# Kernel optimization log

Measured on AMD Instinct MI355X. Metric: run time of the kernel, lower is better.

Reference implementation:

```python
import jax, jax.numpy as jnp
import numpy as np
import math
from itertools import product

IMG = 300
FMAPS = [38, 19, 10, 5, 3, 1]
STEPS = [8, 16, 32, 64, 100, 300]
MINS = [30, 60, 111, 162, 213, 264]
MAXS = [60, 111, 162, 213, 264, 315]
ARS = [[2, 3]] * 6
CHANS = [512, 1024, 512, 256, 256, 256]
NUM_CLASSES = 21
V0, V1 = 0.1, 0.2  # box-encoding variances


def build_priors():
    # faithful port of PriorsBox.forward (runs once, tiny config loop)
    mean = []
    for k, f in enumerate(FMAPS):
        for i, j in product(range(f), repeat=2):
            f_k = IMG / STEPS[k]
            cx = (j + 0.5) / f_k
            cy = (i + 0.5) / f_k
            s_k = MINS[k] / IMG
            mean += [cx, cy, s_k, s_k]
            s_kp = math.sqrt(s_k * (MAXS[k] / IMG))
            mean += [cx, cy, s_kp, s_kp]
            for ar in ARS[k]:
                mean += [cx, cy, s_k * math.sqrt(ar), s_k / math.sqrt(ar)]
                mean += [cx, cy, s_k / math.sqrt(ar), s_k * math.sqrt(ar)]
    p = np.asarray(mean, dtype=np.float32).reshape(-1, 4)
    return np.clip(p, 0.0, 1.0)


def setup_inputs() -> dict:
    key = jax.random.key(0)
    B = 32
    ks = jax.random.split(key, 3 * len(FMAPS))
    inp = {}
    ki = 0
    for s, (C, F) in enumerate(zip(CHANS, FMAPS)):
        inp[f"feat{s}"] = jax.random.normal(ks[ki], (B, C, F, F), jnp.float32); ki += 1
        inp[f"loc_w{s}"] = jax.random.normal(ks[ki], (24, C, 3, 3), jnp.float32) * 0.02; ki += 1
        inp[f"loc_b{s}"] = jnp.zeros((24,), jnp.float32)
        inp[f"conf_w{s}"] = jax.random.normal(ks[ki], (126, C, 3, 3), jnp.float32) * 0.02; ki += 1
        inp[f"conf_b{s}"] = jnp.zeros((126,), jnp.float32)
    inp["priors"] = jnp.asarray(build_priors())  # [11640, 4] cx,cy,w,h
    return inp


def _conv3x3(x, w, b):
    # stride 1, pad 1 -> SAME; NCHW / OIHW layout matches torch Conv2d
    y = jax.lax.conv_general_dilated(x, w, (1, 1), 'SAME',
                                     dimension_numbers=('NCHW', 'OIHW', 'NCHW'))
    return y + b[None, :, None, None]


def _forward(feats, loc_ws, loc_bs, conf_ws, conf_bs, priors):
    B = feats[0].shape[0]
    loc = jnp.concatenate(
        [_conv3x3(x, w, b).transpose(0, 2, 3, 1).reshape(B, -1)
         for x, w, b in zip(feats, loc_ws, loc_bs)], axis=1).reshape(B, -1, 4)
    conf = jnp.concatenate(
        [_conv3x3(x, w, b).transpose(0, 2, 3, 1).reshape(B, -1)
         for x, w, b in zip(feats, conf_ws, conf_bs)], axis=1).reshape(B, -1, NUM_CLASSES)
    scores = jax.nn.softmax(conf, axis=2)
    # decode (vectorized over batch): center-form -> point-form
    p = priors[None]  # [1, P, 4]
    xy = p[..., :2] + loc[..., :2] * V0 * p[..., 2:]
    wh = p[..., 2:] * jnp.exp(loc[..., 2:] * V1)
    mins = xy - wh * 0.5
    boxes = jnp.concatenate([mins, mins + wh], axis=-1)  # [B, P, 4]
    return jnp.concatenate([boxes, scores], axis=-1)  # [B, P, 4 + num_classes]


def reference(feat0, feat1, feat2, feat3, feat4, feat5,
              loc_w0, loc_w1, loc_w2, loc_w3, loc_w4, loc_w5,
              loc_b0, loc_b1, loc_b2, loc_b3, loc_b4, loc_b5,
              conf_w0, conf_w1, conf_w2, conf_w3, conf_w4, conf_w5,
              conf_b0, conf_b1, conf_b2, conf_b3, conf_b4, conf_b5,
              priors):
    feats = (feat0, feat1, feat2, feat3, feat4, feat5)
    loc_ws = (loc_w0, loc_w1, loc_w2, loc_w3, loc_w4, loc_w5)
    loc_bs = (loc_b0, loc_b1, loc_b2, loc_b3, loc_b4, loc_b5)
    conf_ws = (conf_w0, conf_w1, conf_w2, conf_w3, conf_w4, conf_w5)
    conf_bs = (conf_b0, conf_b1, conf_b2, conf_b3, conf_b4, conf_b5)
    return _forward(feats, loc_ws, loc_bs, conf_ws, conf_bs, priors)
```

## Files before the change

### kernel.cpp

```cpp
#include <hip/hip_runtime.h>
#include <hip/hip_bf16.h>
#include <math.h>

typedef __attribute__((ext_vector_type(8))) short bf16x8;
typedef __attribute__((ext_vector_type(16))) float f32x16;

#define NUM_PRIORS 11640
#define OUT_CH 25
#define BATCH 32

#define WT0 0u
#define WT1 1474560u
#define WT2 4423680u
#define WT3 5898240u
#define WT4 6635520u
#define WT5 7372800u
#define XA0 8110080u
#define XA1 60538880u
#define XA2 89440256u
#define XA3 94158848u
#define XA4 94961664u
#define XA5 95371264u
#define CV0 95518720u
#define CV1 125091840u
#define CV2 132485120u
#define CV3 134533120u
#define CV4 135045120u
#define CV5 135229440u
#define WS_TOTAL 135249920u

template <int C>
__device__ __forceinline__
void wprep_body(int idx, const float* lw, const float* cw, unsigned short* wt)
{
  if (idx >= 1440 * C) return;
  constexpr int CK = C / 64;
  const int j    = idx & 7;
  const int lane = (idx >> 3) & 63;
  int rest = idx >> 9;
  const int nt  = rest % 5;  rest /= 5;
  const int ks  = rest & 3;  rest >>= 2;
  const int ck  = rest % CK;
  const int tap = rest / CK;
  const int n = nt * 32 + (lane & 31);
  const int c = ck * 64 + ks * 16 + (lane >> 5) * 8 + j;
  float v = 0.f;
  if (n < 24)       v = lw[((size_t)n        * C + c) * 9 + tap];
  else if (n < 150) v = cw[((size_t)(n - 24) * C + c) * 9 + tap];
  __hip_bfloat16 h = __float2bfloat16(v);
  wt[idx] = *(unsigned short*)&h;
}

template <int C, int F>
__device__ __forceinline__
void xprep_body(int idx, const float* __restrict__ x, unsigned short* __restrict__ xp)
{
  constexpr int P = F + 2, IMGP = P * P, C8 = C / 8, FF = F * F;
  const int pos = idx % IMGP;
  const int bg  = idx / IMGP;
  const int g   = bg % C8;
  const int b   = bg / C8;
  const int py  = pos / P, px = pos % P;
  uint4 out = {0u, 0u, 0u, 0u};
  if (py >= 1 && py <= F && px >= 1 && px <= F) {
    const float* s = x + (((size_t)(b * C + g * 8) * F + (py - 1)) * F + (px - 1));
    unsigned int u[4];
    #pragma unroll
    for (int k = 0; k < 4; ++k) {
      __hip_bfloat162 h = __float22bfloat162_rn(
          float2{s[(size_t)(2 * k) * FF], s[(size_t)(2 * k + 1) * FF]});
      u[k] = *(unsigned int*)&h;
    }
    out.x = u[0]; out.y = u[1]; out.z = u[2]; out.w = u[3];
  }
  *(uint4*)(xp + (size_t)idx * 8) = out;
}

#define XB0 12800
#define XB1 7056
#define XB2 1152
#define XB3 196
#define XB4 100
#define XB5 36
#define WB0 2880
#define WB1 5760
#define WB2 2880
#define WB3 1440
#define WB4 1440
#define WB5 1440
#define PB_TOT (XB0+XB1+XB2+XB3+XB4+XB5+WB0+WB1+WB2+WB3+WB4+WB5)

struct PArgs {
  const float* x[6];
  const float* lw[6];
  const float* cw[6];
  unsigned short* xa[6];
  unsigned short* wt[6];
};

__global__ __launch_bounds__(256)
void prep_all(PArgs a)
{
  int blk = blockIdx.x;
  const int t = threadIdx.x;
  if (blk < XB0) { xprep_body<512, 38>(blk * 256 + t, a.x[0], a.xa[0]); return; } blk -= XB0;
  if (blk < XB1) { xprep_body<1024,19>(blk * 256 + t, a.x[1], a.xa[1]); return; } blk -= XB1;
  if (blk < XB2) { xprep_body<512, 10>(blk * 256 + t, a.x[2], a.xa[2]); return; } blk -= XB2;
  if (blk < XB3) { xprep_body<256,  5>(blk * 256 + t, a.x[3], a.xa[3]); return; } blk -= XB3;
  if (blk < XB4) { xprep_body<256,  3>(blk * 256 + t, a.x[4], a.xa[4]); return; } blk -= XB4;
  if (blk < XB5) { xprep_body<256,  1>(blk * 256 + t, a.x[5], a.xa[5]); return; } blk -= XB5;
  if (blk < WB0) { wprep_body<512> (blk * 256 + t, a.lw[0], a.cw[0], a.wt[0]); return; } blk -= WB0;
  if (blk < WB1) { wprep_body<1024>(blk * 256 + t, a.lw[1], a.cw[1], a.wt[1]); return; } blk -= WB1;
  if (blk < WB2) { wprep_body<512> (blk * 256 + t, a.lw[2], a.cw[2], a.wt[2]); return; } blk -= WB2;
  if (blk < WB3) { wprep_body<256> (blk * 256 + t, a.lw[3], a.cw[3], a.wt[3]); return; } blk -= WB3;
  if (blk < WB4) { wprep_body<256> (blk * 256 + t, a.lw[4], a.cw[4], a.wt[4]); return; } blk -= WB4;
                   wprep_body<256> (blk * 256 + t, a.lw[5], a.cw[5], a.wt[5]);
}

#define BSTEP 2880

template <int C, int F>
__device__ __forceinline__
void conv_body(int bid, int tid, const unsigned short* __restrict__ xp,
               const unsigned short* __restrict__ wt, float* __restrict__ cv,
               uint4 (*lB)[BSTEP])
{
  constexpr int FF   = F * F;
  constexpr int MB   = (FF + 255) / 256;
  constexpr int CK   = C / 64;
  constexpr int P    = F + 2;
  constexpr int IMGP = P * P;
  constexpr int C8   = C / 8;
  constexpr int TS   = CK * 10240;
  constexpr int NIT  = CK * 4;

  const int mt = bid % MB;
  const int b  = bid / MB;

  const int wave = tid >> 6, lane = tid & 63;
  const int mw = wave & 3, ng = wave >> 2;
  const int m0 = mt * 256 + mw * 64;
  const int nbase  = ng * 3;
  const int ncount = ng ? 2 : 3;

  const int cm = lane & 31, khalf = lane >> 5;
  int mi0 = m0 + cm;      if (mi0 > FF - 1) mi0 = FF - 1;
  int mi1 = m0 + 32 + cm; if (mi1 > FF - 1) mi1 = FF - 1;
  const int ay0 = mi0 / F, ax0 = mi0 - ay0 * F;
  const int ay1 = mi1 / F, ax1 = mi1 - ay1 * F;
  const int ylo = m0 / F;
  const int yhi = ((m0 + 63 < FF - 1) ? (m0 + 63) : (FF - 1)) / F;

  const unsigned short* xb = xp + ((size_t)b * C8 + khalf) * IMGP * 8;
  const int o0 = ((ay0 + 1) * P + ax0 + 1) * 8;
  const int o1 = ((ay1 + 1) * P + ax1 + 1) * 8;

  f32x16 acc[2][3];
  #pragma unroll
  for (int mf = 0; mf < 2; ++mf)
    #pragma unroll
    for (int nt = 0; nt < 3; ++nt)
      #pragma unroll
      for (int r = 0; r < 16; ++r) acc[mf][nt][r] = 0.f;

  auto stage = [&](uint4* buf, int it) {
    const int ck = it >> 2, ks = it & 3;
    const unsigned short* wck = wt + ck * 10240 + ks * 2560;
    #pragma unroll
    for (int r = 0; r < 6; ++r) {
      const int e = r * 512 + tid;
      if (r < 5 || e < BSTEP) {
        const int tap = e / 320;
        const int w   = e - tap * 320;
        __builtin_amdgcn_global_load_lds(
            (const __attribute__((address_space(1))) unsigned int*)(wck + (size_t)tap * TS + w * 8),
            (__attribute__((address_space(3))) unsigned int*)&buf[e], 16, 0, 0);
      }
    }
  };

  stage(lB[0], 0);
  int cur = 0;
  #pragma unroll 1
  for (int it = 0; it < NIT; ++it) {
    __syncthreads();
    if (it + 1 < NIT) stage(lB[cur ^ 1], it + 1);
    const int ck = it >> 2, ks = it & 3;
    const unsigned short* xk = xb + (size_t)(ck * 8 + ks * 2) * IMGP * 8;
    const uint4* bp = lB[cur];
    #pragma unroll
    for (int tap = 0; tap < 9; ++tap) {
      const int dy = tap / 3 - 1, dx = tap % 3 - 1;
      if (ylo + dy >= F || yhi + dy < 0) continue;
      if (F == 1 && dx != 0) continue;
      const int d = (dy * P + dx) * 8;
      const bf16x8 a0 = *(const bf16x8*)(xk + o0 + d);
      const bf16x8 a1 = *(const bf16x8*)(xk + o1 + d);
      #pragma unroll
      for (int nt = 0; nt < 3; ++nt) {
        if (nt < ncount) {
          const uint4 u = bp[tap * 320 + (nbase + nt) * 64 + lane];
          const bf16x8 bf = *(const bf16x8*)&u;
          acc[0][nt] = __builtin_amdgcn_mfma_f32_32x32x16_bf16(a0, bf, acc[0][nt], 0, 0, 0);
          acc[1][nt] = __builtin_amdgcn_mfma_f32_32x32x16_bf16(a1, bf, acc[1][nt], 0, 0, 0);
        }
      }
    }
    cur ^= 1;
  }

  float* cb = cv + (size_t)b * FF * 160;
  #pragma unroll
  for (int mf = 0; mf < 2; ++mf)
    #pragma unroll
    for (int nt = 0; nt < 3; ++nt) {
      if (nt < ncount) {
        const int n = (nbase + nt) * 32 + cm;
        #pragma unroll
        for (int r = 0; r < 16; ++r) {
          const int mm = m0 + mf * 32 + (r & 3) + 8 * (r >> 2) + 4 * khalf;
          if (mm < FF) cb[(size_t)mm * 160 + n] = acc[mf][nt][r];
        }
      }
    }
}

#define G1B 64
#define G0B 192
#define G2B 32
#define G3B 32
#define G4B 32
#define G5B 32
#define GB_TOT (G1B + G0B + G2B + G3B + G4B + G5B)

__global__ __launch_bounds__(512, 2)
void gemm_all(char* wsb)
{
  __shared__ uint4 lB[2][BSTEP];
  int blk = blockIdx.x;
  const int tid = threadIdx.x;
  if (blk < G1B) { conv_body<1024,19>(blk, tid, (const unsigned short*)(wsb + XA1),
                                      (const unsigned short*)(wsb + WT1), (float*)(wsb + CV1), lB); return; }
  blk -= G1B;
  if (blk < G0B) { conv_body<512, 38>(blk, tid, (const unsigned short*)(wsb + XA0),
                                      (const unsigned short*)(wsb + WT0), (float*)(wsb + CV0), lB); return; }
  blk -= G0B;
  if (blk < G2B) { conv_body<512, 10>(blk, tid, (const unsigned short*)(wsb + XA2),
                                      (const unsigned short*)(wsb + WT2), (float*)(wsb + CV2), lB); return; }
  blk -= G2B;
  if (blk < G3B) { conv_body<256,  5>(blk, tid, (const unsigned short*)(wsb + XA3),
                                      (const unsigned short*)(wsb + WT3), (float*)(wsb + CV3), lB); return; }
  blk -= G3B;
  if (blk < G4B) { conv_body<256,  3>(blk, tid, (const unsigned short*)(wsb + XA4),
                                      (const unsigned short*)(wsb + WT4), (float*)(wsb + CV4), lB); return; }
  blk -= G4B;
                   conv_body<256,  1>(blk, tid, (const unsigned short*)(wsb + XA5),
                                      (const unsigned short*)(wsb + WT5), (float*)(wsb + CV5), lB);
}

struct DecArgs {
  const float* lb[6];
  const float* cb[6];
};

template <int F>
__device__ __forceinline__
void dec_one(int local, int b, const float* cvs, const float* lb, const float* cb,
             const float* p4, float* o)
{
  constexpr int FF = F * F;
  const int pos = local / 6;
  const int a   = local - pos * 6;
  const float* strip = cvs + ((size_t)b * FF + pos) * 160;

  float cls[21];
  float mx = -1e30f;
  #pragma unroll
  for (int k = 0; k < 21; ++k) {
    cls[k] = strip[24 + a * 21 + k] + cb[a * 21 + k];
    mx = fmaxf(mx, cls[k]);
  }
  float s = 0.f;
  #pragma unroll
  for (int k = 0; k < 21; ++k) { cls[k] = __expf(cls[k] - mx); s += cls[k]; }
  const float inv = 1.f / s;

  const float l0 = strip[a * 4 + 0] + lb[a * 4 + 0];
  const float l1 = strip[a * 4 + 1] + lb[a * 4 + 1];
  const float l2 = strip[a * 4 + 2] + lb[a * 4 + 2];
  const float l3 = strip[a * 4 + 3] + lb[a * 4 + 3];

  const float px = p4[0], py = p4[1], pw = p4[2], ph = p4[3];
  const float cx = px + l0 * 0.1f * pw;
  const float cy = py + l1 * 0.1f * ph;
  const float w  = pw * __expf(l2 * 0.2f);
  const float h  = ph * __expf(l3 * 0.2f);
  const float minx = cx - 0.5f * w;
  const float miny = cy - 0.5f * h;

  o[0] = minx; o[1] = miny; o[2] = minx + w; o[3] = miny + h;
  #pragma unroll
  for (int k = 0; k < 21; ++k) o[4 + k] = cls[k] * inv;
}

__global__ __launch_bounds__(256)
void decode_k(const char* __restrict__ wsb, DecArgs da,
              const float* __restrict__ priors, float* __restrict__ out)
{
  const int gid = blockIdx.x * 256 + threadIdx.x;
  if (gid >= BATCH * NUM_PRIORS) return;
  const int b  = gid / NUM_PRIORS;
  const int pr = gid - b * NUM_PRIORS;
  float* o = out + (size_t)gid * OUT_CH;
  const float* p4 = priors + (size_t)pr * 4;

  if (pr < 8664)       dec_one<38>(pr,         b, (const float*)(wsb + CV0), da.lb[0], da.cb[0], p4, o);
  else if (pr < 10830) dec_one<19>(pr - 8664,  b, (const float*)(wsb + CV1), da.lb[1], da.cb[1], p4, o);
  else if (pr < 11430) dec_one<10>(pr - 10830, b, (const float*)(wsb + CV2), da.lb[2], da.cb[2], p4, o);
  else if (pr < 11580) dec_one<5> (pr - 11430, b, (const float*)(wsb + CV3), da.lb[3], da.cb[3], p4, o);
  else if (pr < 11634) dec_one<3> (pr - 11580, b, (const float*)(wsb + CV4), da.lb[4], da.cb[4], p4, o);
  else                 dec_one<1> (pr - 11634, b, (const float*)(wsb + CV5), da.lb[5], da.cb[5], p4, o);
}

#define TH 4
#define TW 8
#define NPOS 32
#define NUM_OC 160
#define WS_STRIDE 161
#define OS 33
#define CC 8

union SmemFB {
  struct {
    float patch[CC * (TH + 2) * (TW + 2)];
    float w[9 * CC * WS_STRIDE];
  } st;
  float outbuf[NUM_OC * OS];
};

template <int C, int F>
__global__ __launch_bounds__(256)
void ssd_stage(const float* __restrict__ x,
               const float* __restrict__ loc_w, const float* __restrict__ loc_b,
               const float* __restrict__ conf_w, const float* __restrict__ conf_b,
               const float* __restrict__ priors,
               float* __restrict__ out, int stage_off)
{
  constexpr int nx = (F + TW - 1) / TW;
  constexpr int ny = (F + TH - 1) / TH;
  __shared__ SmemFB smem;

  const int bid = blockIdx.x;
  const int b   = bid / (nx * ny);
  const int rem = bid % (nx * ny);
  const int ty  = rem / nx;
  const int tx  = rem % nx;
  const int x0  = tx * TW;
  const int y0  = ty * TH;

  const int t = threadIdx.x;
  const int g = t & 31;
  const int p = t >> 5;

  float acc[5][TH] = {};

  #pragma unroll 1
  for (int c0 = 0; c0 < C; c0 += CC) {
    __syncthreads();
    for (int i = t; i < CC * (TH + 2) * (TW + 2); i += 256) {
      int c  = i / ((TH + 2) * (TW + 2));
      int r  = i - c * ((TH + 2) * (TW + 2));
      int yy = r / (TW + 2);
      int xx = r - yy * (TW + 2);
      int gy = y0 + yy - 1;
      int gx = x0 + xx - 1;
      float v = 0.f;
      if (gy >= 0 && gy < F && gx >= 0 && gx < F)
        v = x[(((size_t)b * C + (c0 + c)) * F + gy) * F + gx];
      smem.st.patch[i] = v;
    }
    for (int i = t; i < NUM_OC * (CC * 9); i += 256) {
      int oc  = i / (CC * 9);
      int j   = i - oc * (CC * 9);
      int c   = j / 9;
      int tap = j - c * 9;
      float v = 0.f;
      if (oc < 24)        v = loc_w [((size_t)oc        * C + (c0 + c)) * 9 + tap];
      else if (oc < 150)  v = conf_w[((size_t)(oc - 24) * C + (c0 + c)) * 9 + tap];
      smem.st.w[(tap * CC + c) * WS_STRIDE + oc] = v;
    }
    __syncthreads();

    for (int tap = 0; tap < 9; ++tap) {
      const int ky = tap / 3;
      const int kx = tap - ky * 3;
      const int xbase = ky * (TW + 2) + kx + p;
      const int wbase = tap * CC * WS_STRIDE + g;
      #pragma unroll
      for (int c = 0; c < CC; ++c) {
        float xv[TH];
        #pragma unroll
        for (int v = 0; v < TH; ++v)
          xv[v] = smem.st.patch[c * ((TH + 2) * (TW + 2)) + v * (TW + 2) + xbase];
        #pragma unroll
        for (int u = 0; u < 5; ++u) {
          float wv = smem.st.w[wbase + c * WS_STRIDE + u * 32];
          #pragma unroll
          for (int v = 0; v < TH; ++v)
            acc[u][v] += wv * xv[v];
        }
      }
    }
  }

  __syncthreads();
  #pragma unroll
  for (int u = 0; u < 5; ++u) {
    int oc = g + 32 * u;
    float bias = 0.f;
    if (oc < 24)       bias = loc_b[oc];
    else if (oc < 150) bias = conf_b[oc - 24];
    #pragma unroll
    for (int v = 0; v < TH; ++v)
      smem.outbuf[oc * OS + v * TW + p] = acc[u][v] + bias;
  }
  __syncthreads();

  if (t < NPOS * 6) {
    int pos = t / 6;
    int a   = t - pos * 6;
    int lx  = pos & 7;
    int ly  = pos >> 3;
    int gx  = x0 + lx;
    int gy  = y0 + ly;
    if (gx < F && gy < F) {
      float cls[21];
      float m = -1e30f;
      #pragma unroll
      for (int k = 0; k < 21; ++k) {
        cls[k] = smem.outbuf[(24 + a * 21 + k) * OS + pos];
        m = fmaxf(m, cls[k]);
      }
      float s = 0.f;
      #pragma unroll
      for (int k = 0; k < 21; ++k) { cls[k] = __expf(cls[k] - m); s += cls[k]; }
      float inv = 1.f / s;

      float l0 = smem.outbuf[(a * 4 + 0) * OS + pos];
      float l1 = smem.outbuf[(a * 4 + 1) * OS + pos];
      float l2 = smem.outbuf[(a * 4 + 2) * OS + pos];
      float l3 = smem.outbuf[(a * 4 + 3) * OS + pos];

      int prior = stage_off + (gy * F + gx) * 6 + a;
      const float* pr = priors + (size_t)prior * 4;
      float px = pr[0], py = pr[1], pw = pr[2], ph = pr[3];
      float cx = px + l0 * 0.1f * pw;
      float cy = py + l1 * 0.1f * ph;
      float w  = pw * __expf(l2 * 0.2f);
      float h  = ph * __expf(l3 * 0.2f);
      float minx = cx - 0.5f * w;
      float miny = cy - 0.5f * h;

      float* o = out + ((size_t)b * NUM_PRIORS + prior) * OUT_CH;
      o[0] = minx;
      o[1] = miny;
      o[2] = minx + w;
      o[3] = miny + h;
      #pragma unroll
      for (int k = 0; k < 21; ++k)
        o[4 + k] = cls[k] * inv;
    }
  }
}

template <int C, int F>
static void launch_stage_fb(void* const* d_in, int base, const float* priors, float* out,
                            int stage_off, hipStream_t stream) {
  constexpr int nx = (F + TW - 1) / TW;
  constexpr int ny = (F + TH - 1) / TH;
  int blocks = BATCH * nx * ny;
  ssd_stage<C, F><<<blocks, 256, 0, stream>>>(
      (const float*)d_in[base + 0], (const float*)d_in[base + 1], (const float*)d_in[base + 2],
      (const float*)d_in[base + 3], (const float*)d_in[base + 4], priors, out, stage_off);
}

extern "C" void kernel_launch(void* const* d_in, const int* in_sizes, int n_in,
                              void* d_out, int out_size, void* d_ws, size_t ws_size,
                              hipStream_t stream) {
  (void)in_sizes; (void)n_in; (void)out_size;
  const float* priors = (const float*)d_in[30];
  float* out = (float*)d_out;

  if (ws_size < (size_t)WS_TOTAL) {
    launch_stage_fb<512,  38>(d_in,  0, priors, out,     0, stream);
    launch_stage_fb<1024, 19>(d_in,  5, priors, out,  8664, stream);
    launch_stage_fb<512,  10>(d_in, 10, priors, out, 10830, stream);
    launch_stage_fb<256,   5>(d_in, 15, priors, out, 11430, stream);
    launch_stage_fb<256,   3>(d_in, 20, priors, out, 11580, stream);
    launch_stage_fb<256,   1>(d_in, 25, priors, out, 11634, stream);
    return;
  }

  char* wsb = (char*)d_ws;
  static const unsigned wtoff[6] = {WT0, WT1, WT2, WT3, WT4, WT5};
  static const unsigned xaoff[6] = {XA0, XA1, XA2, XA3, XA4, XA5};

  PArgs pa;
  for (int s = 0; s < 6; ++s) {
    pa.x[s]  = (const float*)d_in[5 * s];
    pa.lw[s] = (const float*)d_in[5 * s + 1];
    pa.cw[s] = (const float*)d_in[5 * s + 3];
    pa.xa[s] = (unsigned short*)(wsb + xaoff[s]);
    pa.wt[s] = (unsigned short*)(wsb + wtoff[s]);
  }
  prep_all<<<PB_TOT, 256, 0, stream>>>(pa);

  gemm_all<<<GB_TOT, 512, 0, stream>>>(wsb);

  DecArgs da;
  for (int s = 0; s < 6; ++s) {
    da.lb[s] = (const float*)d_in[5 * s + 2];
    da.cb[s] = (const float*)d_in[5 * s + 4];
  }
  decode_k<<<(BATCH * NUM_PRIORS + 255) / 256, 256, 0, stream>>>((const char*)d_ws, da, priors, out);
}
```

Measured before the change: 490.8 us.

## Stage padded input row window into LDS alongside weights via async loads

```diff
diff --git a/kernel.cpp b/kernel.cpp
--- a/kernel.cpp
+++ b/kernel.cpp
@@ -118,12 +118,14 @@
 }
 
 #define BSTEP 2880
+#define BPAD  3072
+#define APAD  1024
 
 template <int C, int F>
 __device__ __forceinline__
 void conv_body(int bid, int tid, const unsigned short* __restrict__ xp,
                const unsigned short* __restrict__ wt, float* __restrict__ cv,
-               uint4 (*lB)[BSTEP])
+               uint4 (*lB)[BPAD], uint4 (*lA)[APAD])
 {
   constexpr int FF   = F * F;
   constexpr int MB   = (FF + 255) / 256;
@@ -133,6 +135,8 @@
   constexpr int C8   = C / 8;
   constexpr int TS   = CK * 10240;
   constexpr int NIT  = CK * 4;
+  constexpr int AR   = ((255 / F + 4) < P) ? (255 / F + 4) : P;
+  constexpr int ANP  = AR * P;
 
   const int mt = bid % MB;
   const int b  = bid / MB;
@@ -151,9 +155,11 @@
   const int ylo = m0 / F;
   const int yhi = ((m0 + 63 < FF - 1) ? (m0 + 63) : (FF - 1)) / F;
 
-  const unsigned short* xb = xp + ((size_t)b * C8 + khalf) * IMGP * 8;
-  const int o0 = ((ay0 + 1) * P + ax0 + 1) * 8;
-  const int o1 = ((ay1 + 1) * P + ax1 + 1) * 8;
+  const int bylo = (mt * 256) / F;
+  const int wy0  = (bylo < P - AR) ? bylo : (P - AR);
+
+  const int af0 = (khalf * AR + (ay0 + 1 - wy0)) * P + (ax0 + 1);
+  const int af1 = (khalf * AR + (ay1 + 1 - wy0)) * P + (ax1 + 1);
 
   f32x16 acc[2][3];
   #pragma unroll
@@ -163,39 +169,52 @@
       #pragma unroll
       for (int r = 0; r < 16; ++r) acc[mf][nt][r] = 0.f;
 
-  auto stage = [&](uint4* buf, int it) {
-    const int ck = it >> 2, ks = it & 3;
+  auto stage = [&](int buf, int it2) {
+    const int ck = it2 >> 2, ks = it2 & 3;
     const unsigned short* wck = wt + ck * 10240 + ks * 2560;
     #pragma unroll
     for (int r = 0; r < 6; ++r) {
-      const int e = r * 512 + tid;
-      if (r < 5 || e < BSTEP) {
-        const int tap = e / 320;
-        const int w   = e - tap * 320;
-        __builtin_amdgcn_global_load_lds(
-            (const __attribute__((address_space(1))) unsigned int*)(wck + (size_t)tap * TS + w * 8),
-            (__attribute__((address_space(3))) unsigned int*)&buf[e], 16, 0, 0);
-      }
+      const int e  = r * 512 + tid;
+      const int es = (e < BSTEP) ? e : (BSTEP - 1);
+      const int tap = es / 320;
+      const int w   = es - tap * 320;
+      __builtin_amdgcn_global_load_lds(
+          (const __attribute__((address_space(1))) unsigned int*)(wck + (size_t)tap * TS + w * 8),
+          (__attribute__((address_space(3))) unsigned int*)&lB[buf][e], 16, 0, 0);
+    }
+    const unsigned short* xbb = xp + ((size_t)b * C8 + ck * 8 + ks * 2) * IMGP * 8;
+    #pragma unroll
+    for (int r = 0; r < 2; ++r) {
+      const int e  = r * 512 + tid;
+      const int es = (e < 2 * ANP) ? e : (2 * ANP - 1);
+      const int p  = es / ANP;
+      const int rr = es - p * ANP;
+      const int ar = rr / P, ac = rr - ar * P;
+      __builtin_amdgcn_global_load_lds(
+          (const __attribute__((address_space(1))) unsigned int*)
+              (xbb + ((size_t)p * IMGP + (wy0 + ar) * P + ac) * 8),
+          (__attribute__((address_space(3))) unsigned int*)&lA[buf][e], 16, 0, 0);
     }
   };
 
-  stage(lB[0], 0);
-  int cur = 0;
+  stage(0, 0);
   #pragma unroll 1
   for (int it = 0; it < NIT; ++it) {
     __syncthreads();
-    if (it + 1 < NIT) stage(lB[cur ^ 1], it + 1);
-    const int ck = it >> 2, ks = it & 3;
-    const unsigned short* xk = xb + (size_t)(ck * 8 + ks * 2) * IMGP * 8;
-    const uint4* bp = lB[cur];
+    if (it + 1 < NIT) stage((it + 1) & 1, it + 1);
+    const uint4* ap = lA[it & 1];
+    const uint4* bp = lB[it & 1];
+    __builtin_amdgcn_s_setprio(1);
     #pragma unroll
     for (int tap = 0; tap < 9; ++tap) {
       const int dy = tap / 3 - 1, dx = tap % 3 - 1;
       if (ylo + dy >= F || yhi + dy < 0) continue;
       if (F == 1 && dx != 0) continue;
-      const int d = (dy * P + dx) * 8;
-      const bf16x8 a0 = *(const bf16x8*)(xk + o0 + d);
-      const bf16x8 a1 = *(const bf16x8*)(xk + o1 + d);
+      const int d = dy * P + dx;
+      const uint4 ua0 = ap[af0 + d];
+      const uint4 ua1 = ap[af1 + d];
+      const bf16x8 a0 = *(const bf16x8*)&ua0;
+      const bf16x8 a1 = *(const bf16x8*)&ua1;
       #pragma unroll
       for (int nt = 0; nt < 3; ++nt) {
         if (nt < ncount) {
@@ -206,7 +225,7 @@
         }
       }
     }
-    cur ^= 1;
+    __builtin_amdgcn_s_setprio(0);
   }
 
   float* cb = cv + (size_t)b * FF * 160;
@@ -236,26 +255,27 @@
 __global__ __launch_bounds__(512, 2)
 void gemm_all(char* wsb)
 {
-  __shared__ uint4 lB[2][BSTEP];
+  __shared__ uint4 lB[2][BPAD];
+  __shared__ uint4 lA[2][APAD];
   int blk = blockIdx.x;
   const int tid = threadIdx.x;
   if (blk < G1B) { conv_body<1024,19>(blk, tid, (const unsigned short*)(wsb + XA1),
-                                      (const unsigned short*)(wsb + WT1), (float*)(wsb + CV1), lB); return; }
+                                      (const unsigned short*)(wsb + WT1), (float*)(wsb + CV1), lB, lA); return; }
   blk -= G1B;
   if (blk < G0B) { conv_body<512, 38>(blk, tid, (const unsigned short*)(wsb + XA0),
-                                      (const unsigned short*)(wsb + WT0), (float*)(wsb + CV0), lB); return; }
+                                      (const unsigned short*)(wsb + WT0), (float*)(wsb + CV0), lB, lA); return; }
   blk -= G0B;
   if (blk < G2B) { conv_body<512, 10>(blk, tid, (const unsigned short*)(wsb + XA2),
-                                      (const unsigned short*)(wsb + WT2), (float*)(wsb + CV2), lB); return; }
+                                      (const unsigned short*)(wsb + WT2), (float*)(wsb + CV2), lB, lA); return; }
   blk -= G2B;
   if (blk < G3B) { conv_body<256,  5>(blk, tid, (const unsigned short*)(wsb + XA3),
-                                      (const unsigned short*)(wsb + WT3), (float*)(wsb + CV3), lB); return; }
+                                      (const unsigned short*)(wsb + WT3), (float*)(wsb + CV3), lB, lA); return; }
   blk -= G3B;
   if (blk < G4B) { conv_body<256,  3>(blk, tid, (const unsigned short*)(wsb + XA4),
-                                      (const unsigned short*)(wsb + WT4), (float*)(wsb + CV4), lB); return; }
+                                      (const unsigned short*)(wsb + WT4), (float*)(wsb + CV4), lB, lA); return; }
   blk -= G4B;
                    conv_body<256,  1>(blk, tid, (const unsigned short*)(wsb + XA5),
-                                      (const unsigned short*)(wsb + WT5), (float*)(wsb + CV5), lB);
+                                      (const unsigned short*)(wsb + WT5), (float*)(wsb + CV5), lB, lA);
 }
 
 struct DecArgs {
```

Result: faster. 437.6 us (-10.8%).
